# Kernel optimization log

Hardware: AMD Instinct MI355X
Metric: run time of the kernel (lower is better)

The kernel has to match this reference:

```python
import jax, jax.numpy as jnp
import numpy as np

DIM = 1024
H = 16
D = DIM // H  # 64
EPS = 1e-6


def _rmsnorm(x, scale):
    # per-last-dim RMSNorm, computed in fp32 like the torch code
    rms = jax.lax.rsqrt(jnp.mean(x * x, axis=-1, keepdims=True) + EPS)
    return x * rms * scale


def _apply_rope(xq, xk, pe):
    # xq, xk: [B,H,L,D]; pe: [1,1,L,D/2,2,2]
    B, h, L, d = xq.shape
    xq_ = xq.reshape(B, h, L, d // 2, 1, 2)
    xk_ = xk.reshape(B, h, L, d // 2, 1, 2)
    xq_out = pe[..., 0] * xq_[..., 0] + pe[..., 1] * xq_[..., 1]  # [B,H,L,D/2,2]
    xk_out = pe[..., 0] * xk_[..., 0] + pe[..., 1] * xk_[..., 1]
    return xq_out.reshape(B, h, L, d), xk_out.reshape(B, h, L, d)


def setup_inputs() -> dict:
    key = jax.random.key(0)
    ks = jax.random.split(key, 6)
    B, L = 2, 2048
    x = jax.random.normal(ks[0], (B, L, DIM), dtype=jnp.float32)
    pe = jax.random.normal(ks[1], (1, 1, L, D // 2, 2, 2), dtype=jnp.float32)
    qkv_w = jax.random.normal(ks[2], (3 * DIM, DIM), dtype=jnp.float32) * (DIM ** -0.5)
    q_scale = jnp.ones((D,), dtype=jnp.float32)
    k_scale = jnp.ones((D,), dtype=jnp.float32)
    proj_w = jax.random.normal(ks[3], (DIM, DIM), dtype=jnp.float32) * (DIM ** -0.5)
    proj_b = jnp.zeros((DIM,), dtype=jnp.float32)
    return {"x": x, "pe": pe, "qkv_w": qkv_w, "q_scale": q_scale,
            "k_scale": k_scale, "proj_w": proj_w, "proj_b": proj_b}


def reference(x, pe, qkv_w, q_scale, k_scale, proj_w, proj_b):
    B, L, _ = x.shape
    x_c = jnp.clip(jnp.nan_to_num(x, nan=0.0, posinf=0.0, neginf=0.0), -10000.0, 10000.0)
    qkv = x_c @ qkv_w.T  # [B,L,3*DIM] (qkv_bias=False)
    qkv = jnp.nan_to_num(qkv, nan=0.0, posinf=0.0, neginf=0.0)
    # 'B L (K H D) -> K B H L D'
    qkv = qkv.reshape(B, L, 3, H, D).transpose(2, 0, 3, 1, 4)
    q, k, v = qkv[0], qkv[1], qkv[2]  # each [B,H,L,D]
    q = _rmsnorm(q, q_scale)
    k = _rmsnorm(k, k_scale)
    q, k = _apply_rope(q, k, pe)
    # scaled dot product attention (no mask)
    scores = jnp.einsum('bhqd,bhkd->bhqk', q, k) * (D ** -0.5)
    attn = jax.nn.softmax(scores, axis=-1)
    out = jnp.einsum('bhqk,bhkd->bhqd', attn, v)
    out = out.transpose(0, 2, 1, 3).reshape(B, L, H * D)  # 'B H L D -> B L (H D)'
    out = jnp.clip(out, -10000.0, 10000.0)
    return out @ proj_w.T + proj_b
```

## Files before the change

### kernel.cpp

```cpp
#include <hip/hip_runtime.h>
#include <hip/hip_bf16.h>

#define DIMC 1024
#define HEADS 16
#define HD 64
#define BATCH 2
#define SEQ 2048

typedef __bf16 bf16;
typedef __bf16 bf16x4 __attribute__((ext_vector_type(4)));
typedef __bf16 bf16x8 __attribute__((ext_vector_type(8)));
typedef float f32x4 __attribute__((ext_vector_type(4)));

__device__ inline f32x4 mfma_bf16(bf16x8 a, bf16x8 b, f32x4 c) {
    return __builtin_amdgcn_mfma_f32_16x16x32_bf16(a, b, c, 0, 0, 0);
}

__device__ inline void st8(bf16* p, bf16x8 v) {
    *(bf16x4*)p       = *(bf16x4*)&v;
    *(bf16x4*)(p + 4) = *((bf16x4*)&v + 1);
}
__device__ inline bf16x8 ld_frag(const bf16* p) {
    bf16x8 r;
    *(bf16x4*)&r       = *(const bf16x4*)p;
    *((bf16x4*)&r + 1) = *(const bf16x4*)(p + 16);
    return r;
}

__global__ __launch_bounds__(256) void k_prep_x(const float* __restrict__ x,
                                                bf16* __restrict__ xb) {
    int i = blockIdx.x * 256 + threadIdx.x;
    float4 v = ((const float4*)x)[i];
    float a[4] = {v.x, v.y, v.z, v.w};
    bf16x4 o;
#pragma unroll
    for (int j = 0; j < 4; ++j) {
        float f = a[j];
        f = __builtin_isfinite(f) ? fminf(fmaxf(f, -10000.f), 10000.f) : 0.f;
        o[j] = (bf16)f;
    }
    ((bf16x4*)xb)[i] = o;
}

__global__ __launch_bounds__(256) void k_cast(const float* __restrict__ a,
                                              bf16* __restrict__ o) {
    int i = blockIdx.x * 256 + threadIdx.x;
    float4 v = ((const float4*)a)[i];
    bf16x4 r = {(bf16)v.x, (bf16)v.y, (bf16)v.z, (bf16)v.w};
    ((bf16x4*)o)[i] = r;
}

template <bool OUT_BF16, bool BIAS, bool SANITIZE>
__global__ __launch_bounds__(256) void k_gemm_bt(const bf16* __restrict__ A,
                                                 const bf16* __restrict__ Bt,
                                                 void* __restrict__ Cv,
                                                 const float* __restrict__ bias,
                                                 int N, int K) {
    __shared__ bf16 As[128][68];
    __shared__ bf16 Bs[128][68];
    const int t = threadIdx.x;
    const int m0 = blockIdx.y * 128, n0 = blockIdx.x * 128;
    const int w = t >> 6, lane = t & 63;
    const int wm = (w >> 1) * 64, wn = (w & 1) * 64;
    const int lr = lane & 15, lg = lane >> 4;

    f32x4 acc[4][4];
#pragma unroll
    for (int i = 0; i < 4; ++i)
#pragma unroll
        for (int j = 0; j < 4; ++j) acc[i][j] = 0.0f;

    for (int k0 = 0; k0 < K; k0 += 64) {
#pragma unroll
        for (int i = 0; i < 4; ++i) {
            int c = t + i * 256;
            int r = c >> 3, col = (c & 7) * 8;
            bf16x8 av = *(const bf16x8*)(A + (size_t)(m0 + r) * K + k0 + col);
            bf16x8 bv = *(const bf16x8*)(Bt + (size_t)(n0 + r) * K + k0 + col);
            st8(&As[r][col], av);
            st8(&Bs[r][col], bv);
        }
        __syncthreads();
#pragma unroll
        for (int kk = 0; kk < 2; ++kk) {
            bf16x8 af[4], bfr[4];
#pragma unroll
            for (int mi = 0; mi < 4; ++mi)
                af[mi] = ld_frag(&As[wm + mi * 16 + lr][kk * 32 + lg * 4]);
#pragma unroll
            for (int ni = 0; ni < 4; ++ni)
                bfr[ni] = ld_frag(&Bs[wn + ni * 16 + lr][kk * 32 + lg * 4]);
#pragma unroll
            for (int mi = 0; mi < 4; ++mi)
#pragma unroll
                for (int ni = 0; ni < 4; ++ni)
                    acc[mi][ni] = mfma_bf16(af[mi], bfr[ni], acc[mi][ni]);
        }
        __syncthreads();
    }
#pragma unroll
    for (int mi = 0; mi < 4; ++mi) {
#pragma unroll
        for (int ni = 0; ni < 4; ++ni) {
            int col = n0 + wn + ni * 16 + lr;
            float bval = BIAS ? bias[col] : 0.f;
#pragma unroll
            for (int r = 0; r < 4; ++r) {
                int row = m0 + wm + mi * 16 + lg * 4 + r;
                float v = acc[mi][ni][r];
                if (SANITIZE) v = __builtin_isfinite(v) ? v : 0.f;
                v += bval;
                if (OUT_BF16)
                    ((bf16*)Cv)[(size_t)row * N + col] = (bf16)v;
                else
                    ((float*)Cv)[(size_t)row * N + col] = v;
            }
        }
    }
}

__global__ __launch_bounds__(256) void k_post(const bf16* __restrict__ qkvb,
                                              const float* __restrict__ pe,
                                              const float* __restrict__ q_scale,
                                              const float* __restrict__ k_scale,
                                              bf16* __restrict__ qb,
                                              bf16* __restrict__ kb,
                                              bf16* __restrict__ vt) {
    const int lb = blockIdx.x, h = blockIdx.y, b = blockIdx.z;
    const int t = threadIdx.x;
    const int row = t >> 2, sub = t & 3;
    const int l = lb * 64 + row;
    const int d0 = sub * 16;
    const size_t rowbase = ((size_t)(b * SEQ + l)) * (3 * DIMC) + h * HD;
    const size_t bh = (size_t)(b * HEADS + h);

#pragma unroll
    for (int qk = 0; qk < 2; ++qk) {
        const bf16* src = qkvb + rowbase + qk * DIMC + d0;
        const float* sc = qk ? k_scale : q_scale;
        bf16x8 v0 = *(const bf16x8*)src;
        bf16x8 v1 = *(const bf16x8*)(src + 8);
        float vals[16];
        float ss = 0.f;
#pragma unroll
        for (int j = 0; j < 8; ++j) {
            vals[j] = (float)v0[j];
            vals[8 + j] = (float)v1[j];
        }
#pragma unroll
        for (int j = 0; j < 16; ++j) ss += vals[j] * vals[j];
        ss += __shfl_xor(ss, 1, 64);
        ss += __shfl_xor(ss, 2, 64);
        float rms = rsqrtf(ss * (1.f / 64.f) + 1e-6f);
        const float outscale = qk ? 1.0f : 0.125f * 1.44269504088896340736f;
        bf16 ob[16];
#pragma unroll
        for (int j = 0; j < 16; j += 2) {
            int d = d0 + j;
            float e0 = vals[j] * rms * sc[d];
            float e1 = vals[j + 1] * rms * sc[d + 1];
            float4 pv = *(const float4*)(pe + (size_t)l * 128 + (d >> 1) * 4);
            float o0 = pv.x * e0 + pv.y * e1;
            float o1 = pv.z * e0 + pv.w * e1;
            ob[j] = (bf16)(o0 * outscale);
            ob[j + 1] = (bf16)(o1 * outscale);
        }
        bf16* dst = (qk ? kb : qb) + (bh * SEQ + l) * HD + d0;
        *(bf16x8*)dst = *(bf16x8*)&ob[0];
        *(bf16x8*)(dst + 8) = *(bf16x8*)&ob[8];
    }

    __shared__ bf16 vlds[64][68];
    {
        const bf16* src = qkvb + rowbase + 2 * DIMC + d0;
        bf16x8 v0 = *(const bf16x8*)src;
        bf16x8 v1 = *(const bf16x8*)(src + 8);
        st8(&vlds[row][d0], v0);
        st8(&vlds[row][d0 + 8], v1);
    }
    __syncthreads();
    {
        const int d = t >> 2, c0 = (t & 3) * 16;
        bf16 ob[16];
#pragma unroll
        for (int j = 0; j < 16; ++j) ob[j] = vlds[c0 + j][d];
        bf16* dst = vt + (bh * HD + d) * SEQ + lb * 64 + c0;
        *(bf16x8*)dst = *(bf16x8*)&ob[0];
        *(bf16x8*)(dst + 8) = *(bf16x8*)&ob[8];
    }
}

__global__ __launch_bounds__(512) void k_attn(const bf16* __restrict__ Q,
                                              const bf16* __restrict__ Kb,
                                              const bf16* __restrict__ Vt,
                                              bf16* __restrict__ O) {
    __shared__ bf16 Qs[128][68];
    __shared__ bf16 Ks[2][64][68];
    __shared__ bf16 Vs[2][64][68];
    const int qt = blockIdx.x, bh = blockIdx.y;
    const int b = bh >> 4, h = bh & 15;
    const int t = threadIdx.x, w = t >> 6, lane = t & 63;
    const int lr = lane & 15, lg = lane >> 4;
    const size_t baseQK = (size_t)bh * SEQ * HD;
    const size_t baseVt = (size_t)bh * HD * SEQ;

    const int sr = t >> 3, scol = (t & 7) * 8;
#pragma unroll
    for (int i = 0; i < 2; ++i) {
        int c = t + i * 512;
        int r = c >> 3, col = (c & 7) * 8;
        bf16x8 v = *(const bf16x8*)(Q + baseQK + (size_t)(qt * 128 + r) * HD + col);
        st8(&Qs[r][col], v);
    }
    {
        bf16x8 kv = *(const bf16x8*)(Kb + baseQK + (size_t)sr * HD + scol);
        bf16x8 vv = *(const bf16x8*)(Vt + baseVt + (size_t)sr * SEQ + scol);
        st8(&Ks[0][sr][scol], kv);
        st8(&Vs[0][sr][scol], vv);
    }
    __syncthreads();
    bf16x8 qf0 = ld_frag(&Qs[w * 16 + lr][lg * 4]);
    bf16x8 qf1 = ld_frag(&Qs[w * 16 + lr][32 + lg * 4]);

    f32x4 oacc[4];
#pragma unroll
    for (int i = 0; i < 4; ++i) oacc[i] = 0.0f;
    float m_s = -1e30f, l_s = 0.f;

    int cur = 0;
    for (int kt = 0; kt < SEQ / 64; ++kt) {
        bf16x8 kreg, vreg;
        const bool pf = (kt + 1) < SEQ / 64;
        if (pf) {
            kreg = *(const bf16x8*)(Kb + baseQK + (size_t)((kt + 1) * 64 + sr) * HD + scol);
            vreg = *(const bf16x8*)(Vt + baseVt + (size_t)sr * SEQ + (kt + 1) * 64 + scol);
        }
        f32x4 s[4];
#pragma unroll
        for (int nk = 0; nk < 4; ++nk) {
            f32x4 a = 0.0f;
            a = mfma_bf16(ld_frag(&Ks[cur][nk * 16 + lr][lg * 4]), qf0, a);
            a = mfma_bf16(ld_frag(&Ks[cur][nk * 16 + lr][32 + lg * 4]), qf1, a);
            s[nk] = a;
        }
        float tm = fmaxf(fmaxf(s[0][0], s[0][1]), fmaxf(s[0][2], s[0][3]));
#pragma unroll
        for (int nk = 1; nk < 4; ++nk)
            tm = fmaxf(tm, fmaxf(fmaxf(s[nk][0], s[nk][1]),
                                 fmaxf(s[nk][2], s[nk][3])));
        tm = fmaxf(tm, __shfl_xor(tm, 16, 64));
        tm = fmaxf(tm, __shfl_xor(tm, 32, 64));
        float mnew = fmaxf(m_s, tm);
        float alpha = exp2f(m_s - mnew);
        m_s = mnew;
        float rs = 0.f;
#pragma unroll
        for (int nk = 0; nk < 4; ++nk)
#pragma unroll
            for (int r2 = 0; r2 < 4; ++r2) {
                float p = exp2f(s[nk][r2] - mnew);
                s[nk][r2] = p;
                rs += p;
            }
        rs += __shfl_xor(rs, 16, 64);
        rs += __shfl_xor(rs, 32, 64);
        l_s = l_s * alpha + rs;
        bf16x8 pa0, pa1;
#pragma unroll
        for (int j = 0; j < 4; ++j) {
            pa0[j]     = (bf16)s[0][j];
            pa0[4 + j] = (bf16)s[1][j];
            pa1[j]     = (bf16)s[2][j];
            pa1[4 + j] = (bf16)s[3][j];
        }
#pragma unroll
        for (int nd = 0; nd < 4; ++nd)
#pragma unroll
            for (int r2 = 0; r2 < 4; ++r2) oacc[nd][r2] *= alpha;
#pragma unroll
        for (int nd = 0; nd < 4; ++nd) {
            oacc[nd] = mfma_bf16(ld_frag(&Vs[cur][nd * 16 + lr][lg * 4]), pa0, oacc[nd]);
            oacc[nd] = mfma_bf16(ld_frag(&Vs[cur][nd * 16 + lr][32 + lg * 4]), pa1, oacc[nd]);
        }
        if (pf) {
            st8(&Ks[cur ^ 1][sr][scol], kreg);
            st8(&Vs[cur ^ 1][sr][scol], vreg);
        }
        __syncthreads();
        cur ^= 1;
    }
    {
        float inv = 1.f / l_s;
        int q = qt * 128 + w * 16 + lr;
#pragma unroll
        for (int nd = 0; nd < 4; ++nd) {
            bf16x4 ov;
#pragma unroll
            for (int r2 = 0; r2 < 4; ++r2) {
                float v = oacc[nd][r2] * inv;
                v = fminf(fmaxf(v, -10000.f), 10000.f);
                ov[r2] = (bf16)v;
            }
            *(bf16x4*)(O + ((size_t)(b * SEQ + q)) * DIMC + h * HD + nd * 16 + lg * 4) = ov;
        }
    }
}

extern "C" void kernel_launch(void* const* d_in, const int* in_sizes, int n_in,
                              void* d_out, int out_size, void* d_ws, size_t ws_size,
                              hipStream_t stream) {
    const float* x = (const float*)d_in[0];
    const float* pe = (const float*)d_in[1];
    const float* qkv_w = (const float*)d_in[2];
    const float* q_scale = (const float*)d_in[3];
    const float* k_scale = (const float*)d_in[4];
    const float* proj_w = (const float*)d_in[5];
    const float* proj_b = (const float*)d_in[6];
    float* out = (float*)d_out;
    char* ws = (char*)d_ws;

    bf16* xb = (bf16*)(ws);
    bf16* wqkv = (bf16*)(ws + (8u << 20));
    bf16* wproj = (bf16*)(ws + (14u << 20));
    bf16* qkvb = (bf16*)(ws + (16u << 20));
    bf16* ao = (bf16*)(ws + (16u << 20));
    bf16* qb = (bf16*)(ws + (40u << 20));
    bf16* kb = (bf16*)(ws + (48u << 20));
    bf16* vt = (bf16*)(ws + (56u << 20));

    k_prep_x<<<4096, 256, 0, stream>>>(x, xb);
    k_cast<<<3072, 256, 0, stream>>>(qkv_w, wqkv);
    k_cast<<<1024, 256, 0, stream>>>(proj_w, wproj);
    k_gemm_bt<true, false, true>
        <<<dim3(24, 32), 256, 0, stream>>>(xb, wqkv, (void*)qkvb, nullptr, 3072, 1024);
    k_post<<<dim3(32, HEADS, BATCH), 256, 0, stream>>>(qkvb, pe, q_scale, k_scale, qb, kb, vt);
    k_attn<<<dim3(SEQ / 128, BATCH * HEADS), 512, 0, stream>>>(qb, kb, vt, ao);
    k_gemm_bt<false, true, false>
        <<<dim3(8, 32), 256, 0, stream>>>(ao, wproj, (void*)out, proj_b, 1024, 1024);
}
```

Baseline: 161.3 us.

## Lazy softmax rescale, MFMA row-sum, direct Q register load, and MFMA priority hints

```diff
diff --git a/kernel.cpp b/kernel.cpp
--- a/kernel.cpp
+++ b/kernel.cpp
@@ -194,7 +194,6 @@
                                               const bf16* __restrict__ Kb,
                                               const bf16* __restrict__ Vt,
                                               bf16* __restrict__ O) {
-    __shared__ bf16 Qs[128][68];
     __shared__ bf16 Ks[2][64][68];
     __shared__ bf16 Vs[2][64][68];
     const int qt = blockIdx.x, bh = blockIdx.y;
@@ -204,14 +203,11 @@
     const size_t baseQK = (size_t)bh * SEQ * HD;
     const size_t baseVt = (size_t)bh * HD * SEQ;
 
+    const bf16* qp = Q + baseQK + (size_t)(qt * 128 + w * 16 + lr) * HD;
+    bf16x8 qf0 = ld_frag(qp + lg * 4);
+    bf16x8 qf1 = ld_frag(qp + 32 + lg * 4);
+
     const int sr = t >> 3, scol = (t & 7) * 8;
-#pragma unroll
-    for (int i = 0; i < 2; ++i) {
-        int c = t + i * 512;
-        int r = c >> 3, col = (c & 7) * 8;
-        bf16x8 v = *(const bf16x8*)(Q + baseQK + (size_t)(qt * 128 + r) * HD + col);
-        st8(&Qs[r][col], v);
-    }
     {
         bf16x8 kv = *(const bf16x8*)(Kb + baseQK + (size_t)sr * HD + scol);
         bf16x8 vv = *(const bf16x8*)(Vt + baseVt + (size_t)sr * SEQ + scol);
@@ -219,13 +215,16 @@
         st8(&Vs[0][sr][scol], vv);
     }
     __syncthreads();
-    bf16x8 qf0 = ld_frag(&Qs[w * 16 + lr][lg * 4]);
-    bf16x8 qf1 = ld_frag(&Qs[w * 16 + lr][32 + lg * 4]);
+
+    bf16x8 ones;
+#pragma unroll
+    for (int j = 0; j < 8; ++j) ones[j] = (bf16)1.0f;
 
     f32x4 oacc[4];
 #pragma unroll
     for (int i = 0; i < 4; ++i) oacc[i] = 0.0f;
-    float m_s = -1e30f, l_s = 0.f;
+    f32x4 lacc = 0.0f;
+    float m_s = -1e30f;
 
     int cur = 0;
     for (int kt = 0; kt < SEQ / 64; ++kt) {
@@ -235,6 +234,7 @@
             kreg = *(const bf16x8*)(Kb + baseQK + (size_t)((kt + 1) * 64 + sr) * HD + scol);
             vreg = *(const bf16x8*)(Vt + baseVt + (size_t)sr * SEQ + (kt + 1) * 64 + scol);
         }
+        __builtin_amdgcn_s_setprio(1);
         f32x4 s[4];
 #pragma unroll
         for (int nk = 0; nk < 4; ++nk) {
@@ -243,6 +243,7 @@
             a = mfma_bf16(ld_frag(&Ks[cur][nk * 16 + lr][32 + lg * 4]), qf1, a);
             s[nk] = a;
         }
+        __builtin_amdgcn_s_setprio(0);
         float tm = fmaxf(fmaxf(s[0][0], s[0][1]), fmaxf(s[0][2], s[0][3]));
 #pragma unroll
         for (int nk = 1; nk < 4; ++nk)
@@ -250,38 +251,34 @@
                                  fmaxf(s[nk][2], s[nk][3])));
         tm = fmaxf(tm, __shfl_xor(tm, 16, 64));
         tm = fmaxf(tm, __shfl_xor(tm, 32, 64));
-        float mnew = fmaxf(m_s, tm);
-        float alpha = exp2f(m_s - mnew);
-        m_s = mnew;
-        float rs = 0.f;
-#pragma unroll
-        for (int nk = 0; nk < 4; ++nk)
-#pragma unroll
-            for (int r2 = 0; r2 < 4; ++r2) {
-                float p = exp2f(s[nk][r2] - mnew);
-                s[nk][r2] = p;
-                rs += p;
-            }
-        rs += __shfl_xor(rs, 16, 64);
-        rs += __shfl_xor(rs, 32, 64);
-        l_s = l_s * alpha + rs;
+        if (!__all(tm <= m_s + 8.f)) {
+            float mnew = fmaxf(m_s, tm);
+            float alpha = exp2f(m_s - mnew);
+            m_s = mnew;
+#pragma unroll
+            for (int nd = 0; nd < 4; ++nd)
+#pragma unroll
+                for (int r2 = 0; r2 < 4; ++r2) oacc[nd][r2] *= alpha;
+#pragma unroll
+            for (int r2 = 0; r2 < 4; ++r2) lacc[r2] *= alpha;
+        }
         bf16x8 pa0, pa1;
 #pragma unroll
         for (int j = 0; j < 4; ++j) {
-            pa0[j]     = (bf16)s[0][j];
-            pa0[4 + j] = (bf16)s[1][j];
-            pa1[j]     = (bf16)s[2][j];
-            pa1[4 + j] = (bf16)s[3][j];
-        }
-#pragma unroll
-        for (int nd = 0; nd < 4; ++nd)
-#pragma unroll
-            for (int r2 = 0; r2 < 4; ++r2) oacc[nd][r2] *= alpha;
+            pa0[j]     = (bf16)exp2f(s[0][j] - m_s);
+            pa0[4 + j] = (bf16)exp2f(s[1][j] - m_s);
+            pa1[j]     = (bf16)exp2f(s[2][j] - m_s);
+            pa1[4 + j] = (bf16)exp2f(s[3][j] - m_s);
+        }
+        __builtin_amdgcn_s_setprio(1);
+        lacc = mfma_bf16(ones, pa0, lacc);
+        lacc = mfma_bf16(ones, pa1, lacc);
 #pragma unroll
         for (int nd = 0; nd < 4; ++nd) {
             oacc[nd] = mfma_bf16(ld_frag(&Vs[cur][nd * 16 + lr][lg * 4]), pa0, oacc[nd]);
             oacc[nd] = mfma_bf16(ld_frag(&Vs[cur][nd * 16 + lr][32 + lg * 4]), pa1, oacc[nd]);
         }
+        __builtin_amdgcn_s_setprio(0);
         if (pf) {
             st8(&Ks[cur ^ 1][sr][scol], kreg);
             st8(&Vs[cur ^ 1][sr][scol], vreg);
@@ -290,7 +287,7 @@
         cur ^= 1;
     }
     {
-        float inv = 1.f / l_s;
+        float inv = 1.f / lacc[0];
         int q = qt * 128 + w * 16 + lr;
 #pragma unroll
         for (int nd = 0; nd < 4; ++nd) {
```

New measurement: 156.3 us. -3.1%, faster.
